# Optimization experiments

Hardware: AMD Instinct MI355X
Metric: run time of the kernel (lower is better)

The kernel has to match this reference:

```python
import jax, jax.numpy as jnp
import numpy as np

B, S, D, H = 8, 512, 1024, 16
HD = D // H                      # head_dim = 64
MAX_SEQ_LEN = 512
SCRATCH_SLOTS = 64


def _rope_cache():
    inv_freq = 1.0 / (10000.0 ** (jnp.arange(0, HD, 2, dtype=jnp.float32) / HD))
    t = jnp.arange(MAX_SEQ_LEN + SCRATCH_SLOTS, dtype=jnp.float32)
    freqs = jnp.outer(t, inv_freq)               # [T, HD//2]
    freqs = jnp.concatenate([freqs, freqs], -1)  # [T, HD]
    return jnp.sin(freqs), jnp.cos(freqs)


def rotate_half(x):
    x1, x2 = x[..., : x.shape[-1] // 2], x[..., x.shape[-1] // 2 :]
    return jnp.concatenate([-x2, x1], axis=-1)


def setup_inputs() -> dict:
    key = jax.random.key(0)
    ks = jax.random.split(key, 5)
    def w(k):
        return jax.random.normal(k, (D, D), dtype=jnp.float32) * 0.02
    return {
        "x": jax.random.normal(ks[0], (B, S, D), dtype=jnp.float32),
        "Wq": w(ks[1]), "bq": jnp.zeros((D,), jnp.float32),
        "Wk": w(ks[2]), "bk": jnp.zeros((D,), jnp.float32),
        "Wv": w(ks[3]), "bv": jnp.zeros((D,), jnp.float32),
        "Wo": w(ks[4]), "bo": jnp.zeros((D,), jnp.float32),
    }


def reference(x, Wq, bq, Wk, bk, Wv, bv, Wo, bo):
    b, s, d = x.shape
    sin_c, cos_c = _rope_cache()
    scale = jnp.array(HD ** (-0.5), dtype=jnp.float32)

    xh = x.astype(jnp.float16)
    def lin(inp, W, bias):  # nnx.Linear with dtype=fp16: cast params + input to fp16
        return inp @ W.astype(jnp.float16) + bias.astype(jnp.float16)

    q = lin(xh, Wq, bq).reshape(b, s, H, HD)
    k = lin(xh, Wk, bk).reshape(b, s, H, HD)
    v = lin(xh, Wv, bv).reshape(b, s, H, HD)

    sin = sin_c[:s, None, :].astype(jnp.float32)  # [s,1,HD]
    cos = cos_c[:s, None, :].astype(jnp.float32)
    qf = q.astype(jnp.float32)
    kf = k.astype(jnp.float32)
    q = qf * cos + rotate_half(qf) * sin
    k = kf * cos + rotate_half(kf) * sin
    v = v.astype(jnp.float32)
    q = q * scale  # module's explicit scale

    # [b,H,s,HD]
    q, k, v = (t.transpose(0, 2, 1, 3) for t in (q, k, v))

    # jax.nn.dot_product_attention additionally scales by 1/sqrt(HD)
    logits = jnp.einsum("bhqd,bhkd->bhqk", q, k) * scale
    probs = jax.nn.softmax(logits, axis=-1)
    out = jnp.einsum("bhqk,bhkd->bhqd", probs, v)
    out = out.transpose(0, 2, 1, 3).reshape(b, s, d)
    return lin(out.astype(jnp.float16), Wo, bo)
```

## Files before the change

kernel.cpp:

```cpp
#include <hip/hip_runtime.h>

typedef _Float16 half8 __attribute__((ext_vector_type(8)));
typedef _Float16 half4v __attribute__((ext_vector_type(4)));
typedef float f32x4 __attribute__((ext_vector_type(4)));

#define OFF_CS    0u
#define OFF_XH    (1u<<20)
#define OFF_WQKVT (OFF_XH + 8u*1024u*1024u)
#define OFF_WOT   (OFF_WQKVT + 8u*1024u*1024u)
#define OFF_QKV   (OFF_WOT + 2u*1024u*1024u)
#define OFF_ATTN  OFF_WQKVT


__device__ __forceinline__ void gload16(const _Float16* g, _Float16* l) {
  __builtin_amdgcn_global_load_lds((const __attribute__((address_space(1))) void*)g,
                                   (__attribute__((address_space(3))) void*)l, 16, 0, 0);
}

__global__ void prep_k(const float* __restrict__ x,
                       const float* __restrict__ W0, const float* __restrict__ W1,
                       const float* __restrict__ W2, const float* __restrict__ W3,
                       _Float16* __restrict__ xh, _Float16* __restrict__ wqkvt,
                       _Float16* __restrict__ wot, float2* __restrict__ cs) {
  int bid = blockIdx.x, tid = threadIdx.x;
  if (bid < 4096) {
    int i = bid * 256 + tid;
    float4 v = ((const float4*)x)[i];
    half4v h;
    h[0] = (_Float16)v.x; h[1] = (_Float16)v.y; h[2] = (_Float16)v.z; h[3] = (_Float16)v.w;
    *(half4v*)(xh + (size_t)i * 4) = h;
  } else if (bid < 8192) {
    __shared__ float tile[32][33];
    int tb = bid - 4096;
    int z = tb >> 10, t = tb & 1023, by = t >> 5, bx = t & 31;
    const float* W = z == 0 ? W0 : z == 1 ? W1 : z == 2 ? W2 : W3;
    _Float16* Wt = z < 3 ? wqkvt + (size_t)z * 1048576 : wot;
    int r = tid >> 3, c0 = (tid & 7) * 4;
    float4 v = *(const float4*)(W + (size_t)(by * 32 + r) * 1024 + bx * 32 + c0);
    tile[r][c0] = v.x; tile[r][c0 + 1] = v.y; tile[r][c0 + 2] = v.z; tile[r][c0 + 3] = v.w;
    __syncthreads();
    half4v h;
#pragma unroll
    for (int j = 0; j < 4; j++) h[j] = (_Float16)tile[c0 + j][r];
    *(half4v*)(Wt + (size_t)(bx * 32 + r) * 1024 + by * 32 + c0) = h;
  } else {
    int idx = (bid - 8192) * 256 + tid;
    int pos = idx >> 5, j = idx & 31;
    float inv = powf(10000.0f, -(float)j * (1.0f / 32.0f));
    float f = (float)pos * inv;
    cs[idx] = make_float2(cosf(f), sinf(f));
  }
}

__global__ __launch_bounds__(256, 2) void gemm_qkv_k(
    const _Float16* __restrict__ A, const _Float16* __restrict__ Bt,
    const float* __restrict__ b0, const float* __restrict__ b1, const float* __restrict__ b2,
    _Float16* __restrict__ C, const float2* __restrict__ cs) {
  __shared__ _Float16 L[4][2][4096];

  int bid = blockIdx.x;
  int wgid = (bid & 7) * 96 + (bid >> 3);
  int by = wgid / 24, bx = wgid % 24;

  int tid = threadIdx.x, lane = tid & 63, w = tid >> 6;
  int wr = w >> 1, wc = w & 1;
  int arow = lane & 15, ag = lane >> 4;
  int s8 = (((arow & 1) << 2) | ag) ^ ((arow >> 1) & 7);

  int qq = (lane & 7) ^ (lane >> 3);
  int rloc = ((lane >> 3) << 1) + (qq >> 2);
  int gcol = (qq & 3) * 8;

  const _Float16* Ag = A + (size_t)(by * 128 + wr * 64) * 1024;
  const _Float16* Bg = Bt + (size_t)(bx * 128 + wc * 64) * 1024;

  f32x4 acc[4][4] = {};

  auto stage = [&](int t) {
    _Float16* dst = &L[w][t & 1][0];
    int k0 = t * 32;
#pragma unroll
    for (int i = 0; i < 4; i++)
      gload16(Ag + (size_t)(i * 16 + rloc) * 1024 + k0 + gcol, dst + i * 512);
#pragma unroll
    for (int i = 0; i < 4; i++)
      gload16(Bg + (size_t)(i * 16 + rloc) * 1024 + k0 + gcol, dst + 2048 + i * 512);
  };

  stage(0);

  for (int t = 0; t < 32; ++t) {
    if (t < 31) stage(t + 1);
    __builtin_amdgcn_sched_barrier(0);
    if (t < 31) asm volatile("s_waitcnt vmcnt(8)" ::: "memory");
    else        asm volatile("s_waitcnt vmcnt(0)" ::: "memory");
    __builtin_amdgcn_sched_barrier(0);
    const _Float16* Lc = &L[w][t & 1][0];
    half8 a[4], b[4];
#pragma unroll
    for (int m = 0; m < 4; m++) {
      int R = m * 16 + arow;
      a[m] = *(const half8*)&Lc[(R >> 1) * 64 + s8 * 8];
    }
#pragma unroll
    for (int n = 0; n < 4; n++) {
      int R = n * 16 + arow;
      b[n] = *(const half8*)&Lc[2048 + (R >> 1) * 64 + s8 * 8];
    }
    __builtin_amdgcn_s_setprio(1);
#pragma unroll
    for (int m = 0; m < 4; m++)
#pragma unroll
      for (int n = 0; n < 4; n++)
        acc[m][n] = __builtin_amdgcn_mfma_f32_16x16x32_f16(a[m], b[n], acc[m][n], 0, 0, 0);
    __builtin_amdgcn_s_setprio(0);
  }

  int gc0 = bx * 128 + wc * 64;
  const float* bp = gc0 < 1024 ? b0 : (gc0 < 2048 ? b1 : b2);
  float bb_[4];
#pragma unroll
  for (int n = 0; n < 4; n++) bb_[n] = bp[(gc0 & 1023) + n * 16 + arow];

  if (gc0 < 2048) {
    bool isQ = gc0 < 1024;
#pragma unroll
    for (int m = 0; m < 4; m++) {
      int gr = by * 128 + wr * 64 + m * 16 + ag * 4;
#pragma unroll
      for (int r = 0; r < 4; r++) {
        int row = gr + r, pos = row & 511;
#pragma unroll
        for (int n = 0; n < 2; n++) {
          int j = n * 16 + arow;
          float av = (float)(_Float16)(acc[m][n][r] + bb_[n]);
          float bv = (float)(_Float16)(acc[m][n + 2][r] + bb_[n + 2]);
          float2 tt = cs[pos * 32 + j];
          float o0 = av * tt.x - bv * tt.y;
          float o1 = bv * tt.x + av * tt.y;
          if (isQ) { o0 *= 0.015625f; o1 *= 0.015625f; }
          C[(size_t)row * 3072 + gc0 + j]      = (_Float16)o0;
          C[(size_t)row * 3072 + gc0 + j + 32] = (_Float16)o1;
        }
      }
    }
  } else {
#pragma unroll
    for (int m = 0; m < 4; m++) {
      int gr = by * 128 + wr * 64 + m * 16 + ag * 4;
      int bb2 = gr >> 9;
      int st6 = (gr & 511) >> 6;
      int s63 = gr & 63;
#pragma unroll
      for (int n = 0; n < 4; n++) {
        int colh = gc0 - 2048 + n * 16 + arow;
        int h = colh >> 6, hd = colh & 63;
        half4v v4;
#pragma unroll
        for (int r = 0; r < 4; r++) v4[r] = (_Float16)(acc[m][n][r] + bb_[n]);
        size_t addr = ((size_t)(bb2 * 512 + hd * 8 + st6)) * 3072 + 2048 + h * 64 + s63;
        *(half4v*)(C + addr) = v4;
      }
    }
  }
}

__global__ __launch_bounds__(256, 2) void gemm_out_k(
    const _Float16* __restrict__ A, const _Float16* __restrict__ Bt,
    const float* __restrict__ b0, float* __restrict__ Cv) {
  constexpr int BM = 64;
  __shared__ _Float16 Ar[3][BM * 32];
  __shared__ _Float16 Br[3][128 * 32];

  int nwg = gridDim.x, cpx = nwg >> 3;
  int bid = blockIdx.x;
  int wgid = (bid & 7) * cpx + (bid >> 3);
  int by = wgid / 8, bx = wgid % 8;

  int tid = threadIdx.x, lane = tid & 63, w = tid >> 6;
  int wr = w >> 1, wc = w & 1;
  int arow = lane & 15, ag = lane >> 4;
  int s8 = (((arow & 1) << 2) | ag) ^ ((arow >> 1) & 7);

  int qq = (lane & 7) ^ (lane >> 3);
  int rloc = ((lane >> 3) << 1) + (qq >> 2);
  int gcol = (qq & 3) * 8;

  const _Float16* Ag = A + (size_t)(by * BM) * 1024;
  const _Float16* Bg = Bt + (size_t)(bx * 128) * 1024;

  f32x4 acc[2][4] = {};

  auto stage = [&](int t) {
    int slot = t % 3;
    int k0 = t * 32;
    gload16(Ag + (size_t)(w * 16 + rloc) * 1024 + k0 + gcol, &Ar[slot][w * 512]);
#pragma unroll
    for (int i = 0; i < 2; i++) {
      int c = w * 2 + i;
      gload16(Bg + (size_t)(c * 16 + rloc) * 1024 + k0 + gcol, &Br[slot][c * 512]);
    }
  };

  stage(0); stage(1);
  asm volatile("s_waitcnt vmcnt(3)" ::: "memory");
  __builtin_amdgcn_s_barrier();
  __builtin_amdgcn_sched_barrier(0);

  for (int t = 0; t < 32; ++t) {
    if (t < 30) stage(t + 2);
    __builtin_amdgcn_sched_barrier(0);
    const _Float16* Ac = &Ar[t % 3][0];
    const _Float16* Bc = &Br[t % 3][0];
    half8 a[2], b[4];
#pragma unroll
    for (int m = 0; m < 2; m++) {
      int R = wr * 32 + m * 16 + arow;
      a[m] = *(const half8*)&Ac[(R >> 1) * 64 + s8 * 8];
    }
#pragma unroll
    for (int n = 0; n < 4; n++) {
      int R = wc * 64 + n * 16 + arow;
      b[n] = *(const half8*)&Bc[(R >> 1) * 64 + s8 * 8];
    }
    __builtin_amdgcn_s_setprio(1);
#pragma unroll
    for (int m = 0; m < 2; m++)
#pragma unroll
      for (int n = 0; n < 4; n++)
        acc[m][n] = __builtin_amdgcn_mfma_f32_16x16x32_f16(a[m], b[n], acc[m][n], 0, 0, 0);
    __builtin_amdgcn_s_setprio(0);
    __builtin_amdgcn_sched_barrier(0);
    if (t < 30)       asm volatile("s_waitcnt vmcnt(3)" ::: "memory");
    else if (t == 30) asm volatile("s_waitcnt vmcnt(0)" ::: "memory");
    if (t < 31) {
      __builtin_amdgcn_s_barrier();
      __builtin_amdgcn_sched_barrier(0);
    }
  }

#pragma unroll
  for (int m = 0; m < 2; m++) {
    int gr = by * BM + wr * 32 + m * 16 + ag * 4;
#pragma unroll
    for (int n = 0; n < 4; n++) {
      int gc = bx * 128 + wc * 64 + n * 16 + arow;
      float bb = b0[gc];
#pragma unroll
      for (int r = 0; r < 4; r++)
        Cv[(size_t)(gr + r) * 1024 + gc] = (float)(_Float16)(acc[m][n][r] + bb);
    }
  }
}

__global__ __launch_bounds__(256, 2) void attn_k(const _Float16* __restrict__ qkv,
                                                 _Float16* __restrict__ out) {
  int id = blockIdx.x;
  int bh = id & 127, qt = id >> 7;
  int b = bh >> 4, h = bh & 15;
  int tid = threadIdx.x, lane = tid & 63, w = tid >> 6;
  int arow = lane & 15, ag = lane >> 4;

  __shared__ _Float16 Ks[64 * 64];
  __shared__ _Float16 Vs[64 * 64];
  __shared__ _Float16 Pl[4][32][72];

  int qrow0 = b * 512 + qt * 128 + w * 32;
  const _Float16* Qp = qkv + (size_t)qrow0 * 3072 + h * 64;
  half8 qa[2][2];
#pragma unroll
  for (int g = 0; g < 2; g++)
#pragma unroll
    for (int ks = 0; ks < 2; ks++)
      qa[g][ks] = *(const half8*)(Qp + (size_t)(g * 16 + arow) * 3072 + ks * 32 + ag * 8);

  const _Float16* Kb = qkv + (size_t)(b * 512) * 3072 + 1024 + h * 64;

  int srow = lane >> 3;
  int sslot = (lane & 7) ^ srow;
  const _Float16* Ksrc0 = Kb + (size_t)(w * 16 + srow) * 3072 + sslot * 8;
  const _Float16* Vsrc0 = qkv + ((size_t)(b * 512) + (w * 16 + srow) * 8) * 3072
                          + 2048 + h * 64 + sslot * 8;

  int rs = arow & 7;

  float psl[2][4] = {};
  f32x4 oacc[2][4] = {};

  for (int st = 0; st < 8; ++st) {
#pragma unroll
    for (int i = 0; i < 2; i++) {
      gload16(Ksrc0 + (size_t)(st * 64 + i * 8) * 3072, &Ks[(w * 16 + i * 8) * 64]);
      gload16(Vsrc0 + (size_t)(i * 64 + st) * 3072,     &Vs[(w * 16 + i * 8) * 64]);
    }
    __syncthreads();

    f32x4 lg[2][4];
#pragma unroll
    for (int c = 0; c < 4; c++) {
      f32x4 a0 = {}, a1 = {};
#pragma unroll
      for (int ks = 0; ks < 2; ks++) {
        int slot = (ks * 4 + ag) ^ rs;
        half8 kb = *(const half8*)&Ks[(c * 16 + arow) * 64 + slot * 8];
        a0 = __builtin_amdgcn_mfma_f32_16x16x32_f16(qa[0][ks], kb, a0, 0, 0, 0);
        a1 = __builtin_amdgcn_mfma_f32_16x16x32_f16(qa[1][ks], kb, a1, 0, 0, 0);
      }
      lg[0][c] = a0;
      lg[1][c] = a1;
    }
#pragma unroll
    for (int g = 0; g < 2; g++) {
      _Float16 ph[4][4];
#pragma unroll
      for (int r = 0; r < 4; r++)
#pragma unroll
        for (int c = 0; c < 4; c++) {
          float p = __builtin_amdgcn_exp2f(lg[g][c][r] * 1.44269504f);
          psl[g][r] += p;
          ph[c][r] = (_Float16)p;
        }
#pragma unroll
      for (int c = 0; c < 4; c++)
#pragma unroll
        for (int r = 0; r < 4; r++)
          Pl[w][g * 16 + ag * 4 + r][c * 16 + arow] = ph[c][r];
    }
#pragma unroll
    for (int ks = 0; ks < 2; ks++) {
      half8 pa0 = *(const half8*)&Pl[w][arow][ks * 32 + ag * 8];
      half8 pa1 = *(const half8*)&Pl[w][16 + arow][ks * 32 + ag * 8];
#pragma unroll
      for (int c = 0; c < 4; c++) {
        int slot = (ks * 4 + ag) ^ rs;
        half8 vb = *(const half8*)&Vs[(c * 16 + arow) * 64 + slot * 8];
        oacc[0][c] = __builtin_amdgcn_mfma_f32_16x16x32_f16(pa0, vb, oacc[0][c], 0, 0, 0);
        oacc[1][c] = __builtin_amdgcn_mfma_f32_16x16x32_f16(pa1, vb, oacc[1][c], 0, 0, 0);
      }
    }
    __syncthreads();
  }
#pragma unroll
  for (int g = 0; g < 2; g++)
#pragma unroll
    for (int r = 0; r < 4; r++)
#pragma unroll
      for (int d = 1; d < 16; d <<= 1) psl[g][r] += __shfl_xor(psl[g][r], d, 16);
#pragma unroll
  for (int g = 0; g < 2; g++)
#pragma unroll
    for (int c = 0; c < 4; c++)
#pragma unroll
      for (int r = 0; r < 4; r++) {
        float v = oacc[g][c][r] / psl[g][r];
        out[(size_t)(qrow0 + g * 16 + ag * 4 + r) * 1024 + h * 64 + c * 16 + arow] =
            (_Float16)v;
      }
}

extern "C" void kernel_launch(void* const* d_in, const int* in_sizes, int n_in,
                              void* d_out, int out_size, void* d_ws, size_t ws_size,
                              hipStream_t stream) {
  const float* x  = (const float*)d_in[0];
  const float* Wq = (const float*)d_in[1];
  const float* bq = (const float*)d_in[2];
  const float* Wk = (const float*)d_in[3];
  const float* bk = (const float*)d_in[4];
  const float* Wv = (const float*)d_in[5];
  const float* bv = (const float*)d_in[6];
  const float* Wo = (const float*)d_in[7];
  const float* bo = (const float*)d_in[8];

  char* ws = (char*)d_ws;
  float2* cs      = (float2*)(ws + OFF_CS);
  _Float16* xh    = (_Float16*)(ws + OFF_XH);
  _Float16* wqkvt = (_Float16*)(ws + OFF_WQKVT);
  _Float16* wot   = (_Float16*)(ws + OFF_WOT);
  _Float16* qkv   = (_Float16*)(ws + OFF_QKV);
  _Float16* attn  = (_Float16*)(ws + OFF_ATTN);

  prep_k<<<8256, 256, 0, stream>>>(x, Wq, Wk, Wv, Wo, xh, wqkvt, wot, cs);
  gemm_qkv_k<<<768, 256, 0, stream>>>(xh, wqkvt, bq, bk, bv, qkv, cs);
  attn_k<<<512, 256, 0, stream>>>(qkv, attn);
  gemm_out_k<<<512, 256, 0, stream>>>(attn, wot, bo, (float*)d_out);
}
```

Measured before the change: 99.85 us.

## Share LDS tiles across waves in QKV GEMM and shrink output GEMM tiles

The QKV GEMM drops per-wave private LDS buffers, where each wave loaded its own 64-row A and B slices, in favour of a block-shared 3-stage ring of 128x32 A and B tiles with barriers. Each global tile is now loaded once per block instead of twice, which halves global-to-LDS traffic, and the launch bound rises to 3 blocks per CU. The output GEMM moves from 64x128 to 64x64 tiles with a 1024-block grid and a launch bound of 4, for more parallelism and occupancy. The cost is added barrier synchronisation in the QKV kernel and less operand reuse per block in the output GEMM.

```diff
diff --git a/kernel.cpp b/kernel.cpp
--- a/kernel.cpp
+++ b/kernel.cpp
@@ -52,11 +52,12 @@
   }
 }
 
-__global__ __launch_bounds__(256, 2) void gemm_qkv_k(
+__global__ __launch_bounds__(256, 3) void gemm_qkv_k(
     const _Float16* __restrict__ A, const _Float16* __restrict__ Bt,
     const float* __restrict__ b0, const float* __restrict__ b1, const float* __restrict__ b2,
     _Float16* __restrict__ C, const float2* __restrict__ cs) {
-  __shared__ _Float16 L[4][2][4096];
+  __shared__ _Float16 Ar[3][128 * 32];
+  __shared__ _Float16 Br[3][128 * 32];
 
   int bid = blockIdx.x;
   int wgid = (bid & 7) * 96 + (bid >> 3);
@@ -71,41 +72,42 @@
   int rloc = ((lane >> 3) << 1) + (qq >> 2);
   int gcol = (qq & 3) * 8;
 
-  const _Float16* Ag = A + (size_t)(by * 128 + wr * 64) * 1024;
-  const _Float16* Bg = Bt + (size_t)(bx * 128 + wc * 64) * 1024;
+  const _Float16* Ag = A + (size_t)(by * 128) * 1024;
+  const _Float16* Bg = Bt + (size_t)(bx * 128) * 1024;
 
   f32x4 acc[4][4] = {};
 
   auto stage = [&](int t) {
-    _Float16* dst = &L[w][t & 1][0];
+    int slot = t % 3;
     int k0 = t * 32;
 #pragma unroll
-    for (int i = 0; i < 4; i++)
-      gload16(Ag + (size_t)(i * 16 + rloc) * 1024 + k0 + gcol, dst + i * 512);
-#pragma unroll
-    for (int i = 0; i < 4; i++)
-      gload16(Bg + (size_t)(i * 16 + rloc) * 1024 + k0 + gcol, dst + 2048 + i * 512);
+    for (int i = 0; i < 2; i++) {
+      int c = w * 2 + i;
+      gload16(Ag + (size_t)(c * 16 + rloc) * 1024 + k0 + gcol, &Ar[slot][c * 512]);
+      gload16(Bg + (size_t)(c * 16 + rloc) * 1024 + k0 + gcol, &Br[slot][c * 512]);
+    }
   };
 
-  stage(0);
+  stage(0); stage(1);
+  asm volatile("s_waitcnt vmcnt(4)" ::: "memory");
+  __builtin_amdgcn_s_barrier();
+  __builtin_amdgcn_sched_barrier(0);
 
   for (int t = 0; t < 32; ++t) {
-    if (t < 31) stage(t + 1);
+    if (t < 30) stage(t + 2);
     __builtin_amdgcn_sched_barrier(0);
-    if (t < 31) asm volatile("s_waitcnt vmcnt(8)" ::: "memory");
-    else        asm volatile("s_waitcnt vmcnt(0)" ::: "memory");
-    __builtin_amdgcn_sched_barrier(0);
-    const _Float16* Lc = &L[w][t & 1][0];
+    const _Float16* Ac = &Ar[t % 3][0];
+    const _Float16* Bc = &Br[t % 3][0];
     half8 a[4], b[4];
 #pragma unroll
     for (int m = 0; m < 4; m++) {
-      int R = m * 16 + arow;
-      a[m] = *(const half8*)&Lc[(R >> 1) * 64 + s8 * 8];
+      int R = wr * 64 + m * 16 + arow;
+      a[m] = *(const half8*)&Ac[(R >> 1) * 64 + s8 * 8];
     }
 #pragma unroll
     for (int n = 0; n < 4; n++) {
-      int R = n * 16 + arow;
-      b[n] = *(const half8*)&Lc[2048 + (R >> 1) * 64 + s8 * 8];
+      int R = wc * 64 + n * 16 + arow;
+      b[n] = *(const half8*)&Bc[(R >> 1) * 64 + s8 * 8];
     }
     __builtin_amdgcn_s_setprio(1);
 #pragma unroll
@@ -114,6 +116,13 @@
       for (int n = 0; n < 4; n++)
         acc[m][n] = __builtin_amdgcn_mfma_f32_16x16x32_f16(a[m], b[n], acc[m][n], 0, 0, 0);
     __builtin_amdgcn_s_setprio(0);
+    __builtin_amdgcn_sched_barrier(0);
+    if (t < 30)       asm volatile("s_waitcnt vmcnt(4)" ::: "memory");
+    else if (t == 30) asm volatile("s_waitcnt vmcnt(0)" ::: "memory");
+    if (t < 31) {
+      __builtin_amdgcn_s_barrier();
+      __builtin_amdgcn_sched_barrier(0);
+    }
   }
 
   int gc0 = bx * 128 + wc * 64;
@@ -165,17 +174,15 @@
   }
 }
 
-__global__ __launch_bounds__(256, 2) void gemm_out_k(
+__global__ __launch_bounds__(256, 4) void gemm_out_k(
     const _Float16* __restrict__ A, const _Float16* __restrict__ Bt,
     const float* __restrict__ b0, float* __restrict__ Cv) {
-  constexpr int BM = 64;
-  __shared__ _Float16 Ar[3][BM * 32];
-  __shared__ _Float16 Br[3][128 * 32];
-
-  int nwg = gridDim.x, cpx = nwg >> 3;
+  __shared__ _Float16 Ar[3][64 * 32];
+  __shared__ _Float16 Br[3][64 * 32];
+
   int bid = blockIdx.x;
-  int wgid = (bid & 7) * cpx + (bid >> 3);
-  int by = wgid / 8, bx = wgid % 8;
+  int wgid = (bid & 7) * 128 + (bid >> 3);
+  int by = wgid >> 4, bx = wgid & 15;
 
   int tid = threadIdx.x, lane = tid & 63, w = tid >> 6;
   int wr = w >> 1, wc = w & 1;
@@ -186,24 +193,20 @@
   int rloc = ((lane >> 3) << 1) + (qq >> 2);
   int gcol = (qq & 3) * 8;
 
-  const _Float16* Ag = A + (size_t)(by * BM) * 1024;
-  const _Float16* Bg = Bt + (size_t)(bx * 128) * 1024;
-
-  f32x4 acc[2][4] = {};
+  const _Float16* Ag = A + (size_t)(by * 64) * 1024;
+  const _Float16* Bg = Bt + (size_t)(bx * 64) * 1024;
+
+  f32x4 acc[2][2] = {};
 
   auto stage = [&](int t) {
     int slot = t % 3;
     int k0 = t * 32;
     gload16(Ag + (size_t)(w * 16 + rloc) * 1024 + k0 + gcol, &Ar[slot][w * 512]);
-#pragma unroll
-    for (int i = 0; i < 2; i++) {
-      int c = w * 2 + i;
-      gload16(Bg + (size_t)(c * 16 + rloc) * 1024 + k0 + gcol, &Br[slot][c * 512]);
-    }
+    gload16(Bg + (size_t)(w * 16 + rloc) * 1024 + k0 + gcol, &Br[slot][w * 512]);
   };
 
   stage(0); stage(1);
-  asm volatile("s_waitcnt vmcnt(3)" ::: "memory");
+  asm volatile("s_waitcnt vmcnt(2)" ::: "memory");
   __builtin_amdgcn_s_barrier();
   __builtin_amdgcn_sched_barrier(0);
 
@@ -212,26 +215,26 @@
     __builtin_amdgcn_sched_barrier(0);
     const _Float16* Ac = &Ar[t % 3][0];
     const _Float16* Bc = &Br[t % 3][0];
-    half8 a[2], b[4];
+    half8 a[2], b[2];
 #pragma unroll
     for (int m = 0; m < 2; m++) {
       int R = wr * 32 + m * 16 + arow;
       a[m] = *(const half8*)&Ac[(R >> 1) * 64 + s8 * 8];
     }
 #pragma unroll
-    for (int n = 0; n < 4; n++) {
-      int R = wc * 64 + n * 16 + arow;
+    for (int n = 0; n < 2; n++) {
+      int R = wc * 32 + n * 16 + arow;
       b[n] = *(const half8*)&Bc[(R >> 1) * 64 + s8 * 8];
     }
     __builtin_amdgcn_s_setprio(1);
 #pragma unroll
     for (int m = 0; m < 2; m++)
 #pragma unroll
-      for (int n = 0; n < 4; n++)
+      for (int n = 0; n < 2; n++)
         acc[m][n] = __builtin_amdgcn_mfma_f32_16x16x32_f16(a[m], b[n], acc[m][n], 0, 0, 0);
     __builtin_amdgcn_s_setprio(0);
     __builtin_amdgcn_sched_barrier(0);
-    if (t < 30)       asm volatile("s_waitcnt vmcnt(3)" ::: "memory");
+    if (t < 30)       asm volatile("s_waitcnt vmcnt(2)" ::: "memory");
     else if (t == 30) asm volatile("s_waitcnt vmcnt(0)" ::: "memory");
     if (t < 31) {
       __builtin_amdgcn_s_barrier();
@@ -241,10 +244,10 @@
 
 #pragma unroll
   for (int m = 0; m < 2; m++) {
-    int gr = by * BM + wr * 32 + m * 16 + ag * 4;
-#pragma unroll
-    for (int n = 0; n < 4; n++) {
-      int gc = bx * 128 + wc * 64 + n * 16 + arow;
+    int gr = by * 64 + wr * 32 + m * 16 + ag * 4;
+#pragma unroll
+    for (int n = 0; n < 2; n++) {
+      int gc = bx * 64 + wc * 32 + n * 16 + arow;
       float bb = b0[gc];
 #pragma unroll
       for (int r = 0; r < 4; r++)
@@ -382,5 +385,5 @@
   prep_k<<<8256, 256, 0, stream>>>(x, Wq, Wk, Wv, Wo, xh, wqkvt, wot, cs);
   gemm_qkv_k<<<768, 256, 0, stream>>>(xh, wqkvt, bq, bk, bv, qkv, cs);
   attn_k<<<512, 256, 0, stream>>>(qkv, attn);
-  gemm_out_k<<<512, 256, 0, stream>>>(attn, wot, bo, (float*)d_out);
-}
+  gemm_out_k<<<1024, 256, 0, stream>>>(attn, wot, bo, (float*)d_out);
+}
```

Result: faster. 89.18 us (-10.7%).
